# Performance work log

Measured on AMD Instinct MI355X. Metric: run time of the kernel, lower is better.

Reference implementation:

```python
import jax, jax.numpy as jnp
import numpy as np

WIN, SIGMA = 11, 1.5
C1, C2, EPS = 0.01 ** 2, 0.03 ** 2, 1e-8


def _gauss_window(win=WIN, sigma=SIGMA):
    coords = jnp.arange(win, dtype=jnp.float32) - (win - 1) / 2
    g = jnp.exp(-coords ** 2 / (2 * sigma ** 2))
    g = g / g.sum()
    return (g[:, None] * g[None, :])[None, None, :, :]


def setup_inputs() -> dict:
    key = jax.random.key(0)
    k1, k2 = jax.random.split(key)
    N, C, H, W = 32, 1, 512, 512
    x = jax.random.uniform(k1, (N, C, H, W), dtype=jnp.float32)
    y = jax.random.uniform(k2, (N, C, H, W), dtype=jnp.float32)
    w = _gauss_window()
    return {"x": x, "y": y, "w": w}


def _conv(x, w):
    pad = w.shape[-1] // 2
    return jax.lax.conv_general_dilated(
        x, w, window_strides=(1, 1), padding=[(pad, pad), (pad, pad)],
        dimension_numbers=("NCHW", "OIHW", "NCHW"))


def reference(x, y, w):
    w = w.astype(x.dtype)
    n = x.shape[0]
    # One fused conv over all five planes stacked on the batch dim.
    stacked = jnp.concatenate([x, y, x * x, y * y, x * y], axis=0)
    conv = _conv(stacked, w)
    mu_x, mu_y, ex2, ey2, exy = (conv[i * n:(i + 1) * n] for i in range(5))
    mu_x2, mu_y2, mu_xy = mu_x ** 2, mu_y ** 2, mu_x * mu_y
    sig_x2 = ex2 - mu_x2
    sig_y2 = ey2 - mu_y2
    sig_xy = exy - mu_xy
    num = (2 * mu_xy + C1) * (2 * sig_xy + C2)
    den = (mu_x2 + mu_y2 + C1) * (sig_x2 + sig_y2 + C2)
    return jnp.clip(num / (den + EPS), 0.0, 1.0).mean()
```

## Files before the change

kernel.cpp:

```cpp
#include <hip/hip_runtime.h>


typedef float v2f __attribute__((ext_vector_type(2)));

#define IMG_H 512
#define IMG_W 512
#define NIMG  32
#define NT    256
#define RROWS 38
#define NCHNK 14
#define ITERS 48
#define SLOTW 80

#define C1F  1.0e-4f
#define C2F  9.0e-4f
#define EPSF 1.0e-8f

static __device__ __forceinline__ v2f pkfma(float s, v2f a, v2f b) {
    v2f sv = {s, s};
    return __builtin_elementwise_fma(sv, a, b);
}

__global__ __launch_bounds__(NT, 4) void ssim_kernel(
    const float* __restrict__ xg, const float* __restrict__ yg,
    const float* __restrict__ wg, float* __restrict__ out)
{
    const int t    = threadIdx.x;
    const int lane = t & 63;
    const int wv   = t >> 6;
    const int bx   = blockIdx.x;
    const int img  = blockIdx.y;
    const int chnk = bx >> 1;
    const int seg  = ((bx & 1) << 2) | wv;
    const int r0   = chnk * RROWS;
    const int C0   = seg * 64;
    const int cown = C0 + lane;

    const float* xb = xg + (size_t)img * (IMG_H * IMG_W);
    const float* yb = yg + (size_t)img * (IMG_H * IMG_W);

    __shared__ alignas(16) v2f seg3[4][3][SLOTW];
    __shared__ float wredS[4];

    float rs = 0.f;
    if (lane < 11) {
        #pragma unroll
        for (int j = 0; j < 11; ++j) rs += wg[lane * 11 + j];
    }
    float g[11];
    #pragma unroll
    for (int k = 0; k < 11; ++k) {
        int gi = __shfl(__float_as_int(rs), k, 64);
        g[k] = __int_as_float(__builtin_amdgcn_readfirstlane(gi));
    }

    const bool isH  = (lane < 5) || (lane >= 59);
    const int  hcol = (lane < 5) ? (C0 - 5 + lane) : (C0 + 64 + (lane - 59));
    const int  hidx = (lane < 5) ? lane : (lane + 10);

    float px0, py0, hx0, hy0;
    float px1, py1, hx1, hy1;

#define LOADROW(ROW, SUF) do {                                             \
        const int r_ = (ROW);                                              \
        px##SUF = 0.f; py##SUF = 0.f; hx##SUF = 0.f; hy##SUF = 0.f;        \
        if ((unsigned)r_ < IMG_H) {                                        \
            const float* xr = xb + (size_t)r_ * IMG_W;                     \
            const float* yr = yb + (size_t)r_ * IMG_W;                     \
            px##SUF = xr[cown];                                            \
            py##SUF = yr[cown];                                            \
            if (isH && (unsigned)hcol < IMG_W) {                           \
                hx##SUF = xr[hcol];                                        \
                hy##SUF = yr[hcol];                                        \
            }                                                              \
        }                                                                  \
    } while (0)

#define WRITESLOT(SL, SUF) do {                                            \
        v2f sd_ = {px##SUF + py##SUF, px##SUF - py##SUF};                  \
        seg3[wv][(SL)][5 + lane] = sd_;                                    \
        if (isH) {                                                         \
            v2f hsd_ = {hx##SUF + hy##SUF, hx##SUF - hy##SUF};             \
            seg3[wv][(SL)][hidx] = hsd_;                                   \
        }                                                                  \
    } while (0)

    LOADROW(r0 - 5, 0);
    LOADROW(r0 - 4, 1);
    WRITESLOT(0, 0);
    WRITESLOT(1, 1);
    LOADROW(r0 - 3, 0);
    LOADROW(r0 - 2, 1);

    v2f rSD[12], rQ[12];

    float acc = 0.f;

    #pragma unroll 1
    for (int base = 0; base < ITERS; base += 12) {
        #pragma unroll
        for (int s = 0; s < 12; ++s) {
            const int i = base + s;

            v2f e[11];
            #pragma unroll
            for (int j = 0; j < 11; ++j)
                e[j] = seg3[wv][s % 3][lane + j];

            if (i <= ITERS - 3) {
                if (s % 2 == 0) WRITESLOT((s + 2) % 3, 0);
                else            WRITESLOT((s + 2) % 3, 1);
            }

            if (i <= ITERS - 5) {
                if (s % 2 == 0) LOADROW(r0 - 5 + i + 4, 0);
                else            LOADROW(r0 - 5 + i + 4, 1);
            }

            v2f hSD = {0.f, 0.f}, hQ = {0.f, 0.f};
            #pragma unroll
            for (int j = 0; j < 11; ++j) {
                const v2f f = e[j] * e[j];
                hSD = pkfma(g[j], e[j], hSD);
                hQ  = pkfma(g[j], f,    hQ);
            }
            rSD[s] = hSD;
            rQ[s]  = hQ;

            if (i >= 10) {
                const int orow = r0 + i - 10;
                if (orow < IMG_H) {
                    v2f mSD = {0.f, 0.f}, mQ = {0.f, 0.f};
                    #pragma unroll
                    for (int j = 0; j < 11; ++j) {
                        const int sl = (s + 2 + j) % 12;
                        mSD = pkfma(g[j], rSD[sl], mSD);
                        mQ  = pkfma(g[j], rQ[sl],  mQ);
                    }
                    const v2f t2 = mSD * mSD;
                    const float a    = 0.5f  * (t2.x + t2.y);
                    const float muxy = 0.25f * (t2.x - t2.y);
                    const float ep   = 0.5f  * (mQ.x + mQ.y);
                    const float eq   = 0.25f * (mQ.x - mQ.y);
                    const float sxy  = eq - muxy;
                    const float ssum = ep - a;
                    const float num  = fmaf(2.f, muxy, C1F) * fmaf(2.f, sxy, C2F);
                    const float den  = (a + C1F) * (ssum + C2F);
                    float v = num * __builtin_amdgcn_rcpf(den + EPSF);
                    acc += fminf(fmaxf(v, 0.f), 1.f);
                }
            }
        }
    }

    #pragma unroll
    for (int off = 32; off > 0; off >>= 1)
        acc += __shfl_down(acc, off, 64);
    if (lane == 0) wredS[wv] = acc;
    __syncthreads();
    if (t == 0) {
        const float tot = (wredS[0] + wredS[1]) + (wredS[2] + wredS[3]);
        atomicAdd(out, tot * (1.0f / (float)((size_t)NIMG * IMG_H * IMG_W)));
    }
}

extern "C" void kernel_launch(void* const* d_in, const int* in_sizes, int n_in,
                              void* d_out, int out_size, void* d_ws, size_t ws_size,
                              hipStream_t stream) {
    const float* x = (const float*)d_in[0];
    const float* y = (const float*)d_in[1];
    const float* w = (const float*)d_in[2];
    float* out = (float*)d_out;

    hipMemsetAsync(out, 0, sizeof(float), stream);

    dim3 grid(NCHNK * 2, NIMG);
    ssim_kernel<<<grid, dim3(NT), 0, stream>>>(x, y, w, out);
}
```

Measured before the change: 120.6 us.

## Double-buffer LDS row reads and make global row loads branch-free with clamped addresses

Reads for the next row's 11-tap window are prefetched from LDS into a second register set (eA/eB ping-pong) before the current row's horizontal filter runs, so LDS latency is hidden behind compute. Global loads now use clamped row and column indices with select-to-zero instead of branches, and the `i <= ITERS-3/5` guards are dropped, so loads and writes run on every iteration. The launch-bounds occupancy hint is removed, which lets the compiler use more registers. The cost is higher register pressure and some wasted loads and LDS writes past the last needed row. The unguarded writes at the end of the chunk appear to touch only slots that are no longer read.

Result: slower. 129.2 us (+7.2%).

```diff
diff --git a/kernel.cpp b/kernel.cpp
--- a/kernel.cpp
+++ b/kernel.cpp
@@ -21,7 +21,7 @@
     return __builtin_elementwise_fma(sv, a, b);
 }
 
-__global__ __launch_bounds__(NT, 4) void ssim_kernel(
+__global__ __launch_bounds__(NT) void ssim_kernel(
     const float* __restrict__ xg, const float* __restrict__ yg,
     const float* __restrict__ wg, float* __restrict__ out)
 {
@@ -57,22 +57,29 @@
     const bool isH  = (lane < 5) || (lane >= 59);
     const int  hcol = (lane < 5) ? (C0 - 5 + lane) : (C0 + 64 + (lane - 59));
     const int  hidx = (lane < 5) ? lane : (lane + 10);
+    const int  hc   = hcol < 0 ? 0 : (hcol > IMG_W - 1 ? IMG_W - 1 : hcol);
+    const bool hinW = ((unsigned)hcol < IMG_W);
 
     float px0, py0, hx0, hy0;
     float px1, py1, hx1, hy1;
 
 #define LOADROW(ROW, SUF) do {                                             \
-        const int r_ = (ROW);                                              \
-        px##SUF = 0.f; py##SUF = 0.f; hx##SUF = 0.f; hy##SUF = 0.f;        \
-        if ((unsigned)r_ < IMG_H) {                                        \
-            const float* xr = xb + (size_t)r_ * IMG_W;                     \
-            const float* yr = yb + (size_t)r_ * IMG_W;                     \
-            px##SUF = xr[cown];                                            \
-            py##SUF = yr[cown];                                            \
-            if (isH && (unsigned)hcol < IMG_W) {                           \
-                hx##SUF = xr[hcol];                                        \
-                hy##SUF = yr[hcol];                                        \
-            }                                                              \
+        const int r_  = (ROW);                                             \
+        const int rc_ = r_ < 0 ? 0 : (r_ > IMG_H - 1 ? IMG_H - 1 : r_);    \
+        const bool ok_ = ((unsigned)r_ < IMG_H);                           \
+        const float* xr_ = xb + (size_t)rc_ * IMG_W;                       \
+        const float* yr_ = yb + (size_t)rc_ * IMG_W;                       \
+        const float a_ = xr_[cown];                                        \
+        const float b_ = yr_[cown];                                        \
+        px##SUF = ok_ ? a_ : 0.f;                                          \
+        py##SUF = ok_ ? b_ : 0.f;                                          \
+        hx##SUF = 0.f; hy##SUF = 0.f;                                      \
+        if (isH) {                                                         \
+            const float c_ = xr_[hc];                                      \
+            const float d_ = yr_[hc];                                      \
+            const bool hok_ = ok_ && hinW;                                 \
+            hx##SUF = hok_ ? c_ : 0.f;                                     \
+            hy##SUF = hok_ ? d_ : 0.f;                                     \
         }                                                                  \
     } while (0)
 
@@ -92,6 +99,10 @@
     LOADROW(r0 - 3, 0);
     LOADROW(r0 - 2, 1);
 
+    v2f eA[11], eB[11];
+    #pragma unroll
+    for (int j = 0; j < 11; ++j) eA[j] = seg3[wv][0][lane + j];
+
     v2f rSD[12], rQ[12];
 
     float acc = 0.f;
@@ -102,27 +113,29 @@
         for (int s = 0; s < 12; ++s) {
             const int i = base + s;
 
-            v2f e[11];
-            #pragma unroll
-            for (int j = 0; j < 11; ++j)
-                e[j] = seg3[wv][s % 3][lane + j];
-
-            if (i <= ITERS - 3) {
-                if (s % 2 == 0) WRITESLOT((s + 2) % 3, 0);
-                else            WRITESLOT((s + 2) % 3, 1);
+            if (s % 2 == 0) {
+                #pragma unroll
+                for (int j = 0; j < 11; ++j)
+                    eB[j] = seg3[wv][(s + 1) % 3][lane + j];
+            } else {
+                #pragma unroll
+                for (int j = 0; j < 11; ++j)
+                    eA[j] = seg3[wv][(s + 1) % 3][lane + j];
             }
 
-            if (i <= ITERS - 5) {
-                if (s % 2 == 0) LOADROW(r0 - 5 + i + 4, 0);
-                else            LOADROW(r0 - 5 + i + 4, 1);
-            }
+            if (s % 2 == 0) WRITESLOT((s + 2) % 3, 0);
+            else            WRITESLOT((s + 2) % 3, 1);
+
+            if (s % 2 == 0) LOADROW(r0 - 1 + i, 0);
+            else            LOADROW(r0 - 1 + i, 1);
 
             v2f hSD = {0.f, 0.f}, hQ = {0.f, 0.f};
             #pragma unroll
             for (int j = 0; j < 11; ++j) {
-                const v2f f = e[j] * e[j];
-                hSD = pkfma(g[j], e[j], hSD);
-                hQ  = pkfma(g[j], f,    hQ);
+                const v2f ej = (s % 2 == 0) ? eA[j] : eB[j];
+                const v2f f = ej * ej;
+                hSD = pkfma(g[j], ej, hSD);
+                hQ  = pkfma(g[j], f,  hQ);
             }
             rSD[s] = hSD;
             rQ[s]  = hQ;
```
